# Performance work log

Measured on AMD Instinct MI355X. Metric: run time of the kernel, lower is better.

## Reference

```python
import jax, jax.numpy as jnp
import numpy as np


def antideriv_tanh(x):
    # int tanh dx = |x| + log1p(exp(-2|x|)), numerically stable
    ax = jnp.abs(x)
    return ax + jnp.log1p(jnp.exp(-2.0 * ax))


def setup_inputs() -> dict:
    key = jax.random.key(0)
    ks = jax.random.split(key, 9)
    nex, d, m, nTh, r = 16384, 2047, 2048, 4, 10
    dp1 = d + 1
    s_in = 1.0 / np.sqrt(dp1)
    s_m = 1.0 / np.sqrt(m)
    return {
        "x": jax.random.normal(ks[0], (nex, dp1), jnp.float32),
        "A": jax.random.normal(ks[1], (r, dp1), jnp.float32) * s_in,
        "W0": jax.random.normal(ks[2], (m, dp1), jnp.float32) * s_in,   # layers[0].weight
        "b0": jax.random.normal(ks[3], (m,), jnp.float32) * 0.01,
        "Wh": jax.random.normal(ks[4], (nTh - 1, m, m), jnp.float32) * s_m,  # layers[1..nTh-1].weight
        "bh": jax.random.normal(ks[5], (nTh - 1, m), jnp.float32) * 0.01,
        "ww": jax.random.normal(ks[6], (1, m), jnp.float32) * s_m,      # w.weight
        "cw": jax.random.normal(ks[7], (1, dp1), jnp.float32) * s_in,   # c.weight
        "cb": jax.random.normal(ks[8], (1,), jnp.float32) * 0.01,       # c.bias
    }


def reference(x, A, W0, b0, Wh, bh, ww, cw, cb):
    # Phi(x) = w @ N(x) + 0.5 * x^T (A^T A) x + c(x)
    symA = A.T @ A                                   # (d+1, d+1)
    quad = 0.5 * jnp.sum((x @ symA) * x, axis=1, keepdims=True)  # (nex, 1)

    # ResNN: opening layer then nTh-1 residual blocks with step h = 1/(nTh-1)
    n_blocks = Wh.shape[0]                           # nTh - 1
    h = 1.0 / n_blocks
    u = antideriv_tanh(x @ W0.T + b0)                # (nex, m)
    for i in range(n_blocks):                        # fixed small layer count
        u = u + h * antideriv_tanh(u @ Wh[i].T + bh[i])

    return u @ ww.T + quad + x @ cw.T + cb           # (nex, 1)
```

## Files before the change

### kernel.cpp

```cpp
#include <hip/hip_runtime.h>
#include <stdint.h>

typedef unsigned short u16;
typedef _Float16 f16;
typedef _Float16 f16x4 __attribute__((ext_vector_type(4)));
typedef _Float16 f16x8 __attribute__((ext_vector_type(8)));
typedef float f32x4 __attribute__((ext_vector_type(4)));

#define NEX 16384
#define DP1 2048
#define MD 2048
#define RD 10
#define NW (2048u*2048u)
#define BM 128
#define BN 128
#define BK 32
#define NSTEP 64

__device__ __forceinline__ float adtanh(float v) {
  float av = fabsf(v);
  return av + __logf(1.0f + __expf(-2.0f * av));
}
__device__ __forceinline__ void gload16(const void* g, void* l) {
  __builtin_amdgcn_global_load_lds(
      (const __attribute__((address_space(1))) void*)g,
      (__attribute__((address_space(3))) void*)l,
      16, 0, 0);
}

__global__ void k_split_w(const float* __restrict__ W0, const float* __restrict__ Wh,
                          f16* __restrict__ wsW) {
  size_t tid = (size_t)blockIdx.x * blockDim.x + threadIdx.x;
  size_t total4 = (4ull * NW) >> 2;
  size_t stride = (size_t)gridDim.x * blockDim.x;
  for (size_t i = tid; i < total4; i += stride) {
    size_t e = i << 2;
    unsigned layer = (unsigned)(e >> 22);
    unsigned rem = (unsigned)(e & (NW - 1));
    const f32x4* src = (layer == 0)
        ? (const f32x4*)(W0 + rem)
        : (const f32x4*)(Wh + (((size_t)(layer - 1)) << 22) + rem);
    f32x4 v = *src;
    f16x4 hv, lv;
#pragma unroll
    for (int e2 = 0; e2 < 4; ++e2) {
      f16 h = (f16)v[e2];
      hv[e2] = h;
      lv[e2] = (f16)(v[e2] - (float)h);
    }
    *(f16x4*)(wsW + (size_t)(2 * layer) * NW + rem) = hv;
    *(f16x4*)(wsW + (size_t)(2 * layer + 1) * NW + rem) = lv;
  }
}

__global__ void k_rows(const float* __restrict__ x, const float* __restrict__ A,
                       const float* __restrict__ cw, const float* __restrict__ cb,
                       float* __restrict__ rowpart, f16* __restrict__ xh,
                       int row0, int nrows) {
  int wave = threadIdx.x >> 6, lane = threadIdx.x & 63;
  int rloc = blockIdx.x * 4 + wave;
  if (rloc >= nrows) return;
  int grow = row0 + rloc;
  const f32x4* xr = (const f32x4*)(x + (size_t)grow * DP1);
  float acc[11];
#pragma unroll
  for (int i = 0; i < 11; ++i) acc[i] = 0.f;
#pragma unroll
  for (int q = 0; q < 8; ++q) {
    int idx = q * 64 + lane;
    f32x4 xv = xr[idx];
#pragma unroll
    for (int r = 0; r < RD; ++r) {
      f32x4 av = ((const f32x4*)(A + (size_t)r * DP1))[idx];
      acc[r] += xv[0]*av[0] + xv[1]*av[1] + xv[2]*av[2] + xv[3]*av[3];
    }
    f32x4 cv = ((const f32x4*)cw)[idx];
    acc[10] += xv[0]*cv[0] + xv[1]*cv[1] + xv[2]*cv[2] + xv[3]*cv[3];
    f16x4 hv;
#pragma unroll
    for (int e = 0; e < 4; ++e) hv[e] = (f16)xv[e];
    *(f16x4*)(xh + (size_t)rloc * DP1 + (size_t)idx * 4) = hv;
  }
#pragma unroll
  for (int i = 0; i < 11; ++i)
#pragma unroll
    for (int s = 32; s > 0; s >>= 1) acc[i] += __shfl_xor(acc[i], s, 64);
  if (lane == 0) {
    float quad = 0.f;
#pragma unroll
    for (int r = 0; r < RD; ++r) quad += acc[r] * acc[r];
    rowpart[grow] = 0.5f * quad + acc[10] + cb[0];
  }
}

__global__ __launch_bounds__(256) void k_gemm(
    const f16* __restrict__ Ah,
    const f16* __restrict__ Bh, const f16* __restrict__ Bl,
    const float* __restrict__ bias,
    const f16* __restrict__ Up, f16* __restrict__ O,
    int resmode) {
  __shared__ f16 sA[2][BM * BK];
  __shared__ f16 sB[2][2][BN * BK];
  int t = threadIdx.x;

  unsigned nwg = gridDim.x;
  unsigned bid = blockIdx.x;
  unsigned qq = nwg >> 3, rr8 = nwg & 7;
  unsigned xcd = bid & 7, idx8 = bid >> 3;
  unsigned swz = (xcd < rr8 ? xcd * (qq + 1) : rr8 * (qq + 1) + (xcd - rr8) * qq) + idx8;
  int bm = swz >> 4, bn = swz & 15;
  int rowA0 = bm * BM, rowB0 = bn * BN;

  f32x4 acc[4][4];
#pragma unroll
  for (int m = 0; m < 4; ++m)
#pragma unroll
    for (int n = 0; n < 4; ++n) acc[m][n] = (f32x4)0.f;

  int lane = t & 63, w = t >> 6;
  int wm = w >> 1, wn = w & 1;
  int fr = lane & 15, kb = lane >> 4;

  auto stage = [&](int buf, int s) {
    int k0 = s * BK;
    int r = t >> 2;
    int innerb = (t & 3) << 4;
#pragma unroll
    for (int q = 0; q < 2; ++q) {
      int rr = q * 64 + r;
      int kbyte = innerb ^ (((rr >> 1) & 3) << 4);
      const char* ga  = (const char*)(Ah + (size_t)(rowA0 + rr) * DP1 + k0) + kbyte;
      const char* gbh = (const char*)(Bh + (size_t)(rowB0 + rr) * DP1 + k0) + kbyte;
      const char* gbl = (const char*)(Bl + (size_t)(rowB0 + rr) * DP1 + k0) + kbyte;
      char* la  = (char*)(&sA[buf][0])    + q * 4096 + w * 1024;
      char* lbh = (char*)(&sB[buf][0][0]) + q * 4096 + w * 1024;
      char* lbl = (char*)(&sB[buf][1][0]) + q * 4096 + w * 1024;
      gload16(ga,  la);
      gload16(gbh, lbh);
      gload16(gbl, lbl);
    }
  };

  stage(0, 0);
  __syncthreads();

  int cur = 0;
  for (int s = 0; s < NSTEP; ++s) {
    if (s + 1 < NSTEP) stage(cur ^ 1, s + 1);
    const char* pa  = (const char*)&sA[cur][0];
    const char* pbh = (const char*)&sB[cur][0][0];
    const char* pbl = (const char*)&sB[cur][1][0];
    f16x8 fa[4], fbh[4], fbl[4];
#pragma unroll
    for (int m = 0; m < 4; ++m) {
      int row = wm * 64 + m * 16 + fr;
      int off = row * 64 + ((kb * 16) ^ (((row >> 1) & 3) << 4));
      fa[m] = *(const f16x8*)(pa + off);
    }
#pragma unroll
    for (int n = 0; n < 4; ++n) {
      int row = wn * 64 + n * 16 + fr;
      int off = row * 64 + ((kb * 16) ^ (((row >> 1) & 3) << 4));
      fbh[n] = *(const f16x8*)(pbh + off);
      fbl[n] = *(const f16x8*)(pbl + off);
    }
#pragma unroll
    for (int m = 0; m < 4; ++m)
#pragma unroll
      for (int n = 0; n < 4; ++n)
        acc[m][n] = __builtin_amdgcn_mfma_f32_16x16x32_f16(fa[m], fbh[n], acc[m][n], 0, 0, 0);
#pragma unroll
    for (int m = 0; m < 4; ++m)
#pragma unroll
      for (int n = 0; n < 4; ++n)
        acc[m][n] = __builtin_amdgcn_mfma_f32_16x16x32_f16(fa[m], fbl[n], acc[m][n], 0, 0, 0);
    __syncthreads();
    cur ^= 1;
  }

  const float H = 1.0f / 3.0f;
#pragma unroll
  for (int m = 0; m < 4; ++m) {
#pragma unroll
    for (int n = 0; n < 4; ++n) {
      int gcol = rowB0 + wn * 64 + n * 16 + fr;
      float bcol = bias[gcol];
#pragma unroll
      for (int j = 0; j < 4; ++j) {
        int grow = rowA0 + wm * 64 + m * 16 + (lane >> 4) * 4 + j;
        size_t off = (size_t)grow * MD + gcol;
        float v = acc[m][n][j] + bcol;
        float act = adtanh(v);
        float val;
        if (resmode) {
          val = (float)Up[off] + H * act;
        } else {
          val = act;
        }
        O[off] = (f16)val;
      }
    }
  }
}

__global__ void k_final(const f16* __restrict__ U,
                        const float* __restrict__ ww, const float* __restrict__ rowpart,
                        float* __restrict__ out, int row0, int nrows) {
  int wave = threadIdx.x >> 6, lane = threadIdx.x & 63;
  int rloc = blockIdx.x * 4 + wave;
  if (rloc >= nrows) return;
  int grow = row0 + rloc;
  const f16x8* ur = (const f16x8*)(U + (size_t)rloc * MD);
  float acc = 0.f;
#pragma unroll
  for (int q = 0; q < 4; ++q) {
    int idx = q * 64 + lane;
    f16x8 uv = ur[idx];
    const f32x4* wp = (const f32x4*)(ww + (size_t)idx * 8);
    f32x4 w0 = wp[0], w1 = wp[1];
#pragma unroll
    for (int e = 0; e < 4; ++e) acc += (float)uv[e] * w0[e];
#pragma unroll
    for (int e = 0; e < 4; ++e) acc += (float)uv[4 + e] * w1[e];
  }
#pragma unroll
  for (int s = 32; s > 0; s >>= 1) acc += __shfl_xor(acc, s, 64);
  if (lane == 0) out[grow] = acc + rowpart[grow];
}

extern "C" void kernel_launch(void* const* d_in, const int* in_sizes, int n_in,
                              void* d_out, int out_size, void* d_ws, size_t ws_size,
                              hipStream_t stream) {
  const float* x  = (const float*)d_in[0];
  const float* A  = (const float*)d_in[1];
  const float* W0 = (const float*)d_in[2];
  const float* b0 = (const float*)d_in[3];
  const float* Wh = (const float*)d_in[4];
  const float* bh = (const float*)d_in[5];
  const float* ww = (const float*)d_in[6];
  const float* cw = (const float*)d_in[7];
  const float* cb = (const float*)d_in[8];
  float* out = (float*)d_out;

  char* ws = (char*)d_ws;
  f16* wsW = (f16*)ws;
  size_t offRP = 4ull * 2 * NW * 2;
  float* rowpart = (float*)(ws + offRP);
  size_t offSets = offRP + (size_t)NEX * 4;

  int chunkM = 16384;
  while (chunkM > 128 && offSets + 2ull * (size_t)chunkM * 4096 > ws_size) chunkM >>= 1;

  f16* s0 = (f16*)(ws + offSets);
  f16* s1 = (f16*)(ws + offSets + (size_t)chunkM * 4096);

  k_split_w<<<2048, 256, 0, stream>>>(W0, Wh, wsW);

  for (int row0 = 0; row0 < NEX; row0 += chunkM) {
    int nrows = NEX - row0 < chunkM ? NEX - row0 : chunkM;
    int gblocks = (nrows / BM) * (MD / BN);
    int rblocks = (nrows + 3) / 4;
    k_rows<<<rblocks, 256, 0, stream>>>(x, A, cw, cb, rowpart, s0, row0, nrows);
    k_gemm<<<gblocks, 256, 0, stream>>>(s0, wsW + 0ull*NW, wsW + 1ull*NW, b0,
                                        nullptr, s1, 0);
    k_gemm<<<gblocks, 256, 0, stream>>>(s1, wsW + 2ull*NW, wsW + 3ull*NW, bh + 0*MD,
                                        s1, s0, 1);
    k_gemm<<<gblocks, 256, 0, stream>>>(s0, wsW + 4ull*NW, wsW + 5ull*NW, bh + 1*MD,
                                        s0, s1, 1);
    k_gemm<<<gblocks, 256, 0, stream>>>(s1, wsW + 6ull*NW, wsW + 7ull*NW, bh + 2*MD,
                                        s1, s0, 1);
    k_final<<<rblocks, 256, 0, stream>>>(s0, ww, rowpart, out, row0, nrows);
  }
}
```

Before: 1.667 ms.

## Enlarge GEMM tiles to 256x256 with 4-stage LDS pipeline and split-K over hi/lo

The GEMM now uses 256x256 output tiles with 512 threads (8 waves, each computing 128x64) and 128 KB of dynamic LDS holding a 4-buffer, prefetch-distance-2 pipeline driven by explicit vmcnt waits and raw barriers. The hi and lo weight halves are handled as 128 sequential K tiles instead of being loaded together per step, which halves the B staging per tile. It also adds s_setprio around the MFMA blocks. The goal is more data reuse per LDS/global load and better overlap of loads with compute. The cost is higher register pressure and LDS use that limit occupancy, and fewer, larger workgroups that may tail poorly.

New measurement: 1.502 ms. 1.11x faster.

```diff
diff --git a/kernel.cpp b/kernel.cpp
--- a/kernel.cpp
+++ b/kernel.cpp
@@ -1,7 +1,6 @@
 #include <hip/hip_runtime.h>
 #include <stdint.h>
 
-typedef unsigned short u16;
 typedef _Float16 f16;
 typedef _Float16 f16x4 __attribute__((ext_vector_type(4)));
 typedef _Float16 f16x8 __attribute__((ext_vector_type(8)));
@@ -12,10 +11,10 @@
 #define MD 2048
 #define RD 10
 #define NW (2048u*2048u)
-#define BM 128
-#define BN 128
+#define BM 256
+#define BN 256
 #define BK 32
-#define NSTEP 64
+#define KTILES 128
 
 __device__ __forceinline__ float adtanh(float v) {
   float av = fabsf(v);
@@ -93,14 +92,15 @@
   }
 }
 
-__global__ __launch_bounds__(256) void k_gemm(
+__global__ __launch_bounds__(512, 2) void k_gemm(
     const f16* __restrict__ Ah,
     const f16* __restrict__ Bh, const f16* __restrict__ Bl,
     const float* __restrict__ bias,
     const f16* __restrict__ Up, f16* __restrict__ O,
     int resmode) {
-  __shared__ f16 sA[2][BM * BK];
-  __shared__ f16 sB[2][2][BN * BK];
+  extern __shared__ char smem[];
+  char* sAb = smem;
+  char* sBb = smem + 65536;
   int t = threadIdx.x;
 
   unsigned nwg = gridDim.x;
@@ -108,95 +108,97 @@
   unsigned qq = nwg >> 3, rr8 = nwg & 7;
   unsigned xcd = bid & 7, idx8 = bid >> 3;
   unsigned swz = (xcd < rr8 ? xcd * (qq + 1) : rr8 * (qq + 1) + (xcd - rr8) * qq) + idx8;
-  int bm = swz >> 4, bn = swz & 15;
+  int bm = swz >> 3, bn = swz & 7;
   int rowA0 = bm * BM, rowB0 = bn * BN;
 
-  f32x4 acc[4][4];
-#pragma unroll
-  for (int m = 0; m < 4; ++m)
+  int lane = t & 63, w = t >> 6;
+  int wm = w >> 2, wn = w & 3;
+  int fr = lane & 15, kb = lane >> 4;
+
+  f32x4 acc[8][4];
+#pragma unroll
+  for (int m = 0; m < 8; ++m)
 #pragma unroll
     for (int n = 0; n < 4; ++n) acc[m][n] = (f32x4)0.f;
 
-  int lane = t & 63, w = t >> 6;
-  int wm = w >> 1, wn = w & 1;
-  int fr = lane & 15, kb = lane >> 4;
-
-  auto stage = [&](int buf, int s) {
-    int k0 = s * BK;
-    int r = t >> 2;
-    int innerb = (t & 3) << 4;
-#pragma unroll
-    for (int q = 0; q < 2; ++q) {
-      int rr = q * 64 + r;
-      int kbyte = innerb ^ (((rr >> 1) & 3) << 4);
-      const char* ga  = (const char*)(Ah + (size_t)(rowA0 + rr) * DP1 + k0) + kbyte;
-      const char* gbh = (const char*)(Bh + (size_t)(rowB0 + rr) * DP1 + k0) + kbyte;
-      const char* gbl = (const char*)(Bl + (size_t)(rowB0 + rr) * DP1 + k0) + kbyte;
-      char* la  = (char*)(&sA[buf][0])    + q * 4096 + w * 1024;
-      char* lbh = (char*)(&sB[buf][0][0]) + q * 4096 + w * 1024;
-      char* lbl = (char*)(&sB[buf][1][0]) + q * 4096 + w * 1024;
-      gload16(ga,  la);
-      gload16(gbh, lbh);
-      gload16(gbl, lbl);
+  int srow = t >> 2;
+  int sslot = t & 3;
+
+  auto stage = [&](int kt) {
+    int buf = kt & 3;
+    const f16* Bsrc = (kt < 64) ? Bh : Bl;
+    int k0 = (kt & 63) * BK;
+#pragma unroll
+    for (int g = 0; g < 2; ++g) {
+      int row = g * 128 + srow;
+      int sl = sslot ^ ((row >> 1) & 3);
+      const char* ga = (const char*)(Ah   + (size_t)(rowA0 + row) * DP1 + k0) + sl * 16;
+      const char* gb = (const char*)(Bsrc + (size_t)(rowB0 + row) * DP1 + k0) + sl * 16;
+      char* la = sAb + buf * 16384 + g * 8192 + w * 1024;
+      char* lb = sBb + buf * 16384 + g * 8192 + w * 1024;
+      gload16(ga, la);
+      gload16(gb, lb);
     }
   };
 
-  stage(0, 0);
-  __syncthreads();
-
-  int cur = 0;
-  for (int s = 0; s < NSTEP; ++s) {
-    if (s + 1 < NSTEP) stage(cur ^ 1, s + 1);
-    const char* pa  = (const char*)&sA[cur][0];
-    const char* pbh = (const char*)&sB[cur][0][0];
-    const char* pbl = (const char*)&sB[cur][1][0];
-    f16x8 fa[4], fbh[4], fbl[4];
-#pragma unroll
-    for (int m = 0; m < 4; ++m) {
-      int row = wm * 64 + m * 16 + fr;
-      int off = row * 64 + ((kb * 16) ^ (((row >> 1) & 3) << 4));
-      fa[m] = *(const f16x8*)(pa + off);
-    }
+  stage(0);
+  stage(1);
+  asm volatile("s_waitcnt vmcnt(4)" ::: "memory");
+  __builtin_amdgcn_s_barrier();
+
+  for (int kt = 0; kt < KTILES; ++kt) {
+    if (kt + 2 < KTILES) stage(kt + 2);
+    const char* pa = sAb + (kt & 3) * 16384;
+    const char* pb = sBb + (kt & 3) * 16384;
+    f16x8 fb[4], fa[4];
 #pragma unroll
     for (int n = 0; n < 4; ++n) {
       int row = wn * 64 + n * 16 + fr;
-      int off = row * 64 + ((kb * 16) ^ (((row >> 1) & 3) << 4));
-      fbh[n] = *(const f16x8*)(pbh + off);
-      fbl[n] = *(const f16x8*)(pbl + off);
-    }
-#pragma unroll
-    for (int m = 0; m < 4; ++m)
+      fb[n] = *(const f16x8*)(pb + row * 64 + ((kb ^ ((row >> 1) & 3)) << 4));
+    }
+#pragma unroll
+    for (int i = 0; i < 4; ++i) {
+      int row = wm * 128 + i * 16 + fr;
+      fa[i] = *(const f16x8*)(pa + row * 64 + ((kb ^ ((row >> 1) & 3)) << 4));
+    }
+    __builtin_amdgcn_s_setprio(1);
+#pragma unroll
+    for (int i = 0; i < 4; ++i)
 #pragma unroll
       for (int n = 0; n < 4; ++n)
-        acc[m][n] = __builtin_amdgcn_mfma_f32_16x16x32_f16(fa[m], fbh[n], acc[m][n], 0, 0, 0);
-#pragma unroll
-    for (int m = 0; m < 4; ++m)
+        acc[i][n] = __builtin_amdgcn_mfma_f32_16x16x32_f16(fa[i], fb[n], acc[i][n], 0, 0, 0);
+    __builtin_amdgcn_s_setprio(0);
+#pragma unroll
+    for (int i = 0; i < 4; ++i) {
+      int row = wm * 128 + (4 + i) * 16 + fr;
+      fa[i] = *(const f16x8*)(pa + row * 64 + ((kb ^ ((row >> 1) & 3)) << 4));
+    }
+    __builtin_amdgcn_s_setprio(1);
+#pragma unroll
+    for (int i = 0; i < 4; ++i)
 #pragma unroll
       for (int n = 0; n < 4; ++n)
-        acc[m][n] = __builtin_amdgcn_mfma_f32_16x16x32_f16(fa[m], fbl[n], acc[m][n], 0, 0, 0);
-    __syncthreads();
-    cur ^= 1;
+        acc[4 + i][n] = __builtin_amdgcn_mfma_f32_16x16x32_f16(fa[i], fb[n], acc[4 + i][n], 0, 0, 0);
+    __builtin_amdgcn_s_setprio(0);
+    if (kt + 2 < KTILES) asm volatile("s_waitcnt vmcnt(4)" ::: "memory");
+    else                 asm volatile("s_waitcnt vmcnt(0)" ::: "memory");
+    __builtin_amdgcn_s_barrier();
   }
 
   const float H = 1.0f / 3.0f;
 #pragma unroll
-  for (int m = 0; m < 4; ++m) {
+  for (int m = 0; m < 8; ++m) {
 #pragma unroll
     for (int n = 0; n < 4; ++n) {
       int gcol = rowB0 + wn * 64 + n * 16 + fr;
       float bcol = bias[gcol];
 #pragma unroll
       for (int j = 0; j < 4; ++j) {
-        int grow = rowA0 + wm * 64 + m * 16 + (lane >> 4) * 4 + j;
+        int grow = rowA0 + wm * 128 + m * 16 + (lane >> 4) * 4 + j;
         size_t off = (size_t)grow * MD + gcol;
         float v = acc[m][n][j] + bcol;
         float act = adtanh(v);
-        float val;
-        if (resmode) {
-          val = (float)Up[off] + H * act;
-        } else {
-          val = act;
-        }
+        float val = resmode ? ((float)Up[off] + H * act) : act;
         O[off] = (f16)val;
       }
     }
@@ -249,10 +251,13 @@
   size_t offSets = offRP + (size_t)NEX * 4;
 
   int chunkM = 16384;
-  while (chunkM > 128 && offSets + 2ull * (size_t)chunkM * 4096 > ws_size) chunkM >>= 1;
+  while (chunkM > 256 && offSets + 2ull * (size_t)chunkM * 4096 > ws_size) chunkM >>= 1;
 
   f16* s0 = (f16*)(ws + offSets);
   f16* s1 = (f16*)(ws + offSets + (size_t)chunkM * 4096);
+
+  hipFuncSetAttribute((const void*)k_gemm,
+                      hipFuncAttributeMaxDynamicSharedMemorySize, 131072);
 
   k_split_w<<<2048, 256, 0, stream>>>(W0, Wh, wsW);
 
@@ -261,14 +266,14 @@
     int gblocks = (nrows / BM) * (MD / BN);
     int rblocks = (nrows + 3) / 4;
     k_rows<<<rblocks, 256, 0, stream>>>(x, A, cw, cb, rowpart, s0, row0, nrows);
-    k_gemm<<<gblocks, 256, 0, stream>>>(s0, wsW + 0ull*NW, wsW + 1ull*NW, b0,
-                                        nullptr, s1, 0);
-    k_gemm<<<gblocks, 256, 0, stream>>>(s1, wsW + 2ull*NW, wsW + 3ull*NW, bh + 0*MD,
-                                        s1, s0, 1);
-    k_gemm<<<gblocks, 256, 0, stream>>>(s0, wsW + 4ull*NW, wsW + 5ull*NW, bh + 1*MD,
-                                        s0, s1, 1);
-    k_gemm<<<gblocks, 256, 0, stream>>>(s1, wsW + 6ull*NW, wsW + 7ull*NW, bh + 2*MD,
-                                        s1, s0, 1);
+    k_gemm<<<gblocks, 512, 131072, stream>>>(s0, wsW + 0ull*NW, wsW + 1ull*NW, b0,
+                                             nullptr, s1, 0);
+    k_gemm<<<gblocks, 512, 131072, stream>>>(s1, wsW + 2ull*NW, wsW + 3ull*NW, bh + 0*MD,
+                                             s1, s0, 1);
+    k_gemm<<<gblocks, 512, 131072, stream>>>(s0, wsW + 4ull*NW, wsW + 5ull*NW, bh + 1*MD,
+                                             s0, s1, 1);
+    k_gemm<<<gblocks, 512, 131072, stream>>>(s1, wsW + 6ull*NW, wsW + 7ull*NW, bh + 2*MD,
+                                             s1, s0, 1);
     k_final<<<rblocks, 256, 0, stream>>>(s0, ww, rowpart, out, row0, nrows);
   }
 }
```
